# Kernel optimization log

Hardware: AMD Instinct MI355X
Metric: run time of the kernel (lower is better)

The kernel has to match this reference:

```python
import jax, jax.numpy as jnp
import numpy as np

STATE_LEN = 128
SEQ_LEN = 2048  # middle segment length; total T = SEQ_LEN + 2*STATE_LEN = 2304


def _l2norm(t):
    # matches torch F.normalize(p=2, dim=-1, eps=1e-12)
    n = jnp.sqrt(jnp.sum(t * t, axis=-1, keepdims=True))
    return t / jnp.maximum(n, 1e-12)


def setup_inputs() -> dict:
    key = jax.random.key(0)
    ks = jax.random.split(key, 8)
    B, D, H, dk, dv = 1, 1024, 16, 64, 64
    T = SEQ_LEN + 2 * STATE_LEN
    x = jax.random.normal(ks[0], (B, T, D), dtype=jnp.float32)
    w = lambda k, do: jax.random.normal(k, (H, D, do), dtype=jnp.float32) * 0.02
    return {
        "x": x,
        "Wq": w(ks[1], dk),
        "Wk": w(ks[2], dk),
        "Wv": w(ks[3], dv),
        "Wq_state": w(ks[4], dk),
        "Wk_state": w(ks[5], dk),
        "Wv_state": w(ks[6], dv),
        "scaling_factor": jnp.full((H,), 1.0 / np.sqrt(dk), dtype=jnp.float32),
    }


def reference(x, Wq, Wk, Wv, Wq_state, Wk_state, Wv_state, scaling_factor):
    sl, seq = STATE_LEN, SEQ_LEN
    # extract_state: [start_state | sequence | end_state]
    x0 = x[:, :sl]
    xm = x[:, sl:sl + seq]
    x1 = x[:, sl + seq:]

    proj = lambda t, W: jnp.einsum('bsd,hdk->bhsk', t, W)  # StackedLinear, no bias

    q = jnp.concatenate([_l2norm(proj(x0, Wq_state)), _l2norm(proj(xm, Wq)), _l2norm(proj(x1, Wq_state))], axis=2)
    k = jnp.concatenate([_l2norm(proj(x0, Wk_state)), _l2norm(proj(xm, Wk)), _l2norm(proj(x1, Wk_state))], axis=2)
    v = jnp.concatenate([_l2norm(proj(x0, Wv_state)), _l2norm(proj(xm, Wv)), _l2norm(proj(x1, Wv_state))], axis=2)

    T = q.shape[2]
    row = jnp.arange(T)[:, None]
    col = jnp.arange(T)[None, :]
    allowed = col <= row  # causal (tril, diagonal=0)
    # end-state rows may not attend to start-state cols (attn_bias[..., seq+sl:seq+2sl, :sl] = 0 before log)
    allowed = allowed & ~((row >= sl + seq) & (col < sl))
    mask = jnp.where(allowed, 0.0, -jnp.inf).astype(q.dtype)  # log of 0/1 tril

    # per-head learnable scale applied to q@k^T, then additive mask, softmax, @v
    scores = jnp.einsum('bhqd,bhkd->bhqk', q, k) * scaling_factor[None, :, None, None] + mask
    att = jax.nn.softmax(scores, axis=-1)
    return jnp.einsum('bhqk,bhkd->bhqd', att, v)
```

## Files before the change

### kernel.cpp

```cpp
#include <hip/hip_runtime.h>
#include <hip/hip_bf16.h>

#define T_TOT 2304
#define DDIM  1024
#define NH    16
#define DK    64
#define SLEN  128
#define SEQ   2048

typedef __bf16 bf16x8 __attribute__((ext_vector_type(8)));
typedef __bf16 bf16x4 __attribute__((ext_vector_type(4)));
typedef float  f32x4  __attribute__((ext_vector_type(4)));
typedef float  f32x16 __attribute__((ext_vector_type(16)));

__device__ __forceinline__ void async_copy16(const void* gsrc, void* ldst) {
  __builtin_amdgcn_global_load_lds(
      (const __attribute__((address_space(1))) void*)gsrc,
      (__attribute__((address_space(3))) void*)ldst, 16, 0, 0);
}

__device__ __forceinline__ void lds_barrier() {
  __asm__ volatile("s_waitcnt lgkmcnt(0)\n\ts_barrier" ::: "memory");
}

__global__ __launch_bounds__(256) void convert_kernel(
    const float* __restrict__ x,
    const float* __restrict__ Wq, const float* __restrict__ Wk,
    const float* __restrict__ Wv, const float* __restrict__ Wqs,
    const float* __restrict__ Wks, const float* __restrict__ Wvs,
    __bf16* __restrict__ xb, __bf16* __restrict__ Wt) {
  const int b = blockIdx.x;
  const int tid = threadIdx.x;
  if (b < 576) {
    const float4* xin = (const float4*)x;
#pragma unroll
    for (int it = 0; it < 4; ++it) {
      int idx4 = b * 1024 + it * 256 + tid;
      float4 v = xin[idx4];
      bf16x4 o;
      o[0] = (__bf16)v.x; o[1] = (__bf16)v.y; o[2] = (__bf16)v.z; o[3] = (__bf16)v.w;
      *(bf16x4*)(xb + (size_t)idx4 * 4) = o;
    }
    return;
  }
  __shared__ float tile[64 * 65];
  const int wb = b - 576;
  const int m  = wb >> 8;
  const int rem = wb & 255;
  const int h  = rem >> 4;
  const int dt = rem & 15;
  const int d0 = dt * 64;
  const float* Wsrc = (m == 0 ? Wq : m == 1 ? Wk : m == 2 ? Wv
                      : m == 3 ? Wqs : m == 4 ? Wks : Wvs) + (size_t)h * (DDIM * DK);
#pragma unroll
  for (int rr = 0; rr < 4; ++rr) {
    int drow = rr * 16 + (tid >> 4);
    int nc   = (tid & 15) * 4;
    float4 v = *(const float4*)(Wsrc + (size_t)(d0 + drow) * DK + nc);
    tile[(nc + 0) * 65 + drow] = v.x;
    tile[(nc + 1) * 65 + drow] = v.y;
    tile[(nc + 2) * 65 + drow] = v.z;
    tile[(nc + 3) * 65 + drow] = v.w;
  }
  __syncthreads();
  {
    int n  = tid >> 2;
    int rg = (tid & 3) * 16;
    __bf16* dst = Wt + (((size_t)(m * NH + h)) * DK + n) * DDIM + d0 + rg;
    bf16x8 o0, o1;
#pragma unroll
    for (int e = 0; e < 8; e++) o0[e] = (__bf16)tile[n * 65 + rg + e];
#pragma unroll
    for (int e = 0; e < 8; e++) o1[e] = (__bf16)tile[n * 65 + rg + 8 + e];
    *(bf16x8*)dst = o0;
    *(bf16x8*)(dst + 8) = o1;
  }
}

__global__ __launch_bounds__(256) void proj_kernel(
    const __bf16* __restrict__ xb, const __bf16* __restrict__ Wt,
    const float* __restrict__ scal,
    __bf16* __restrict__ qkv, __bf16* __restrict__ vt) {
  const int ntile = blockIdx.x;
  const int rt    = blockIdx.y;
  const int which = blockIdx.z;
  const int r0    = rt * 128;
  const int m     = (rt == 0 || rt == 17) ? which + 3 : which;

  __shared__ __bf16 Xs[128 * 64];
  __shared__ __bf16 Wsh[128 * 64];

  const int tid  = threadIdx.x;
  const int wave = tid >> 6, lane = tid & 63;
  const int quad = lane >> 4, lc = lane & 15;
  const int wr   = wave >> 1, wc = wave & 1;
  const int h    = ntile * 2 + wc;

  const __bf16* Wbase = Wt + ((size_t)m * NH) * (DK * DDIM) + (size_t)(ntile * 128) * DDIM;

  const f32x4 fz = {0.f, 0.f, 0.f, 0.f};
  f32x4 acc[4][4];
#pragma unroll
  for (int i = 0; i < 4; i++)
#pragma unroll
    for (int j = 0; j < 4; j++) acc[i][j] = fz;

  for (int k0 = 0; k0 < DDIM; k0 += 64) {
#pragma unroll
    for (int it = 0; it < 4; ++it) {
      int L = it * 256 + tid;
      int row = L >> 3, c = (L & 7) ^ ((L >> 3) & 7);
      async_copy16(xb + (size_t)(r0 + row) * DDIM + k0 + c * 8,
                   (char*)Xs + (size_t)(it * 256 + wave * 64) * 16);
    }
#pragma unroll
    for (int it = 0; it < 4; ++it) {
      int L = it * 256 + tid;
      int row = L >> 3, c = (L & 7) ^ ((L >> 3) & 7);
      async_copy16(Wbase + (size_t)row * DDIM + k0 + c * 8,
                   (char*)Wsh + (size_t)(it * 256 + wave * 64) * 16);
    }
    __syncthreads();
#pragma unroll
    for (int kk = 0; kk < 2; kk++) {
      bf16x8 afr[4], bfr[4];
#pragma unroll
      for (int i = 0; i < 4; i++) {
        int row = wr * 64 + i * 16 + lc;
        int ch  = (kk * 4 + quad) ^ (row & 7);
        afr[i] = *(const bf16x8*)(Xs + (row * 8 + ch) * 8);
      }
#pragma unroll
      for (int j = 0; j < 4; j++) {
        int row = wc * 64 + j * 16 + lc;
        int ch  = (kk * 4 + quad) ^ (row & 7);
        bfr[j] = *(const bf16x8*)(Wsh + (row * 8 + ch) * 8);
      }
#pragma unroll
      for (int i = 0; i < 4; i++)
#pragma unroll
        for (int j = 0; j < 4; j++)
          acc[i][j] = __builtin_amdgcn_mfma_f32_16x16x32_bf16(afr[i], bfr[j], acc[i][j], 0, 0, 0);
    }
    __syncthreads();
  }

  const float qscale = (which == 0) ? scal[h] * 1.44269504088896f : 1.0f;
  float inv4[4][4];
#pragma unroll
  for (int i = 0; i < 4; i++) {
#pragma unroll
    for (int r = 0; r < 4; r++) {
      float s = 0.f;
#pragma unroll
      for (int j = 0; j < 4; j++) { float v = acc[i][j][r]; s += v * v; }
#pragma unroll
      for (int off = 1; off < 16; off <<= 1) s += __shfl_xor(s, off, 64);
      inv4[i][r] = qscale / fmaxf(sqrtf(s), 1e-12f);
    }
  }
  if (which == 2) {
    __bf16* vtp = vt + (size_t)h * (DK * T_TOT);
#pragma unroll
    for (int i = 0; i < 4; i++) {
      int rowbase = r0 + wr * 64 + i * 16 + quad * 4;
#pragma unroll
      for (int j = 0; j < 4; j++) {
        bf16x4 o;
#pragma unroll
        for (int r = 0; r < 4; r++) o[r] = (__bf16)(acc[i][j][r] * inv4[i][r]);
        *(bf16x4*)(vtp + (size_t)(j * 16 + lc) * T_TOT + rowbase) = o;
      }
    }
  } else {
    __bf16* outp = qkv + ((size_t)(which * NH + h)) * ((size_t)T_TOT * DK);
#pragma unroll
    for (int i = 0; i < 4; i++)
#pragma unroll
      for (int r = 0; r < 4; r++) {
        int row = r0 + wr * 64 + i * 16 + quad * 4 + r;
#pragma unroll
        for (int j = 0; j < 4; j++)
          outp[(size_t)row * DK + j * 16 + lc] = (__bf16)(acc[i][j][r] * inv4[i][r]);
      }
  }
}

__global__ __launch_bounds__(256, 3) void attn_kernel(
    const __bf16* __restrict__ qkv, const __bf16* __restrict__ vt,
    float* __restrict__ Opart, float* __restrict__ Lpart) {
  const int b    = blockIdx.x;
  const int h    = b & 15;
  const int rest = b >> 4;
  const int qg   = 35 - (rest >> 1);
  const int si   = rest & 1;
  const int q0b  = qg * 64;
  const int tid  = threadIdx.x;
  const int wave = tid >> 6, lane = tid & 63;
  const int quad = lane >> 4, lc = lane & 15;
  const int l32  = lane & 31, hi = lane >> 5;

  const __bf16* qp = qkv + ((size_t)h) * ((size_t)T_TOT * DK);
  const __bf16* kp = qkv + ((size_t)(NH + h)) * ((size_t)T_TOT * DK);
  const __bf16* vp = vt + (size_t)h * (DK * T_TOT);

  __shared__ __bf16 Ks[2][64 * 64];
  __shared__ __bf16 Vs[2][64 * 64];
  __shared__ __bf16 Ps[64 * 64];
  __shared__ float  lred[4][64];

  bf16x8 qf[4][2];
#pragma unroll
  for (int qt = 0; qt < 4; qt++)
#pragma unroll
    for (int kk = 0; kk < 2; kk++)
      qf[qt][kk] = *(const bf16x8*)(qp + (size_t)(q0b + qt * 16 + lc) * DK + kk * 32 + quad * 8);

  f32x16 acc_o;
#pragma unroll
  for (int e = 0; e < 16; e++) acc_o[e] = 0.f;
  float lp[4] = {0.f, 0.f, 0.f, 0.f};

  const int jsAll = (q0b >= SLEN + SEQ) ? 2 : 0;
  const int n     = qg - jsAll + 1;
  const int half  = (n + 1) >> 1;
  const int j0    = jsAll + (si ? half : 0);
  const int j1    = si ? qg : (jsAll + half - 1);

  auto stage = [&](int j, int bufi) {
    const __bf16* kT = kp + (size_t)j * 64 * DK;
#pragma unroll
    for (int it = 0; it < 2; ++it) {
      int L = it * 256 + tid;
      int row = L >> 3, c = (L & 7) ^ ((L >> 3) & 7);
      async_copy16(kT + (size_t)row * DK + c * 8,
                   (char*)&Ks[bufi][0] + (size_t)(it * 256 + wave * 64) * 16);
    }
#pragma unroll
    for (int it = 0; it < 2; ++it) {
      int L = it * 256 + tid;
      int d = L >> 3, c = (L & 7) ^ ((L >> 3) & 7);
      async_copy16(vp + (size_t)d * T_TOT + j * 64 + c * 8,
                   (char*)&Vs[bufi][0] + (size_t)(it * 256 + wave * 64) * 16);
    }
  };

  int cur = 0;
  if (j0 <= j1) stage(j0, 0);

  const int d0 = (wave >> 1) * 32;
  const int q0 = (wave & 1) * 32;

  for (int j = j0; j <= j1; ++j) {
    __syncthreads();
    if (j < j1) stage(j + 1, cur ^ 1);

    const bool diag = (j == qg);

    bf16x8 kA[2];
#pragma unroll
    for (int kk = 0; kk < 2; kk++) {
      int row = wave * 16 + lc;
      kA[kk] = *(const bf16x8*)(&Ks[cur][(row * 8 + ((kk * 4 + quad) ^ (lc & 7))) * 8]);
    }
    f32x4 s[4];
#pragma unroll
    for (int qt = 0; qt < 4; qt++) {
      s[qt] = (f32x4){0.f, 0.f, 0.f, 0.f};
#pragma unroll
      for (int kk = 0; kk < 2; kk++)
        s[qt] = __builtin_amdgcn_mfma_f32_16x16x32_bf16(kA[kk], qf[qt][kk], s[qt], 0, 0, 0);
    }

#pragma unroll
    for (int qt = 0; qt < 4; qt++) {
      if (diag) {
#pragma unroll
        for (int r = 0; r < 4; r++)
          if ((wave * 16 + quad * 4 + r) > (qt * 16 + lc)) s[qt][r] = -__builtin_inff();
      }
      bf16x4 pb;
#pragma unroll
      for (int r = 0; r < 4; r++) {
        float pe = exp2f(s[qt][r]);
        lp[qt] += pe;
        pb[r] = (__bf16)pe;
      }
      int el = (qt * 16 + lc) * 64 + (((wave * 2 + (quad >> 1)) ^ (lc & 7)) * 8) + (quad & 1) * 4;
      *(bf16x4*)(&Ps[el]) = pb;
    }

    lds_barrier();

#pragma unroll
    for (int ks = 0; ks < 4; ks++) {
      int ch = (ks * 2 + hi) ^ (l32 & 7);
      bf16x8 vA = *(const bf16x8*)(&Vs[cur][((d0 + l32) * 8 + ch) * 8]);
      bf16x8 pB = *(const bf16x8*)(&Ps[((q0 + l32) * 8 + ch) * 8]);
      acc_o = __builtin_amdgcn_mfma_f32_32x32x16_bf16(vA, pB, acc_o, 0, 0, 0);
    }
    cur ^= 1;
  }

#pragma unroll
  for (int qt = 0; qt < 4; qt++) {
    lp[qt] += __shfl_xor(lp[qt], 16, 64);
    lp[qt] += __shfl_xor(lp[qt], 32, 64);
  }
  lred[wave][quad * 16 + lc] = lp[quad];
  __syncthreads();
  if (wave == 0)
    Lpart[(size_t)b * 64 + lane] = lred[0][lane] + lred[1][lane] + lred[2][lane] + lred[3][lane];

  float* Ob = Opart + (size_t)b * 4096;
  const size_t rowbase = (size_t)(q0 + l32) * DK;
#pragma unroll
  for (int g = 0; g < 4; g++) {
    f32x4 o;
#pragma unroll
    for (int t = 0; t < 4; t++) o[t] = acc_o[g * 4 + t];
    *(f32x4*)(&Ob[rowbase + d0 + 4 * hi + 8 * g]) = o;
  }
}

__global__ __launch_bounds__(256) void combine_kernel(
    const float* __restrict__ Opart, const float* __restrict__ Lpart,
    float* __restrict__ out) {
  const int b  = blockIdx.x;
  const int h  = b & 15;
  const int qg = b >> 4;
  const int b0 = (((35 - qg) * 2) << 4) | h;
  const int b1 = b0 + 16;
  const int tid = threadIdx.x;

  __shared__ float invl[64];
  if (tid < 64)
    invl[tid] = 1.0f / (Lpart[(size_t)b0 * 64 + tid] + Lpart[(size_t)b1 * 64 + tid]);
  __syncthreads();

  const float* O0 = Opart + (size_t)b0 * 4096;
  const float* O1 = Opart + (size_t)b1 * 4096;
  float* op = out + ((size_t)h * T_TOT + qg * 64) * DK;
#pragma unroll
  for (int it = 0; it < 4; ++it) {
    int i4 = it * 256 + tid;
    f32x4 a = *(const f32x4*)(&O0[i4 * 4]);
    f32x4 c = *(const f32x4*)(&O1[i4 * 4]);
    float iv = invl[i4 >> 4];
    f32x4 o;
#pragma unroll
    for (int r = 0; r < 4; r++) o[r] = (a[r] + c[r]) * iv;
    *(f32x4*)(&op[i4 * 4]) = o;
  }
}

extern "C" void kernel_launch(void* const* d_in, const int* in_sizes, int n_in,
                              void* d_out, int out_size, void* d_ws, size_t ws_size,
                              hipStream_t stream) {
  const float* x    = (const float*)d_in[0];
  const float* Wq   = (const float*)d_in[1];
  const float* Wk   = (const float*)d_in[2];
  const float* Wv   = (const float*)d_in[3];
  const float* Wqs  = (const float*)d_in[4];
  const float* Wks  = (const float*)d_in[5];
  const float* Wvs  = (const float*)d_in[6];
  const float* scal = (const float*)d_in[7];
  float* out = (float*)d_out;

  char* ws = (char*)d_ws;
  size_t off = 0;
  __bf16* xb    = (__bf16*)(ws + off); off += (size_t)T_TOT * DDIM * 2;
  __bf16* Wt    = (__bf16*)(ws + off); off += (size_t)6 * NH * DK * DDIM * 2;
  __bf16* qkv   = (__bf16*)(ws + off); off += (size_t)2 * NH * T_TOT * DK * 2;
  __bf16* vt    = (__bf16*)(ws + off); off += (size_t)NH * DK * T_TOT * 2;
  float*  Opart = (float*)(ws + off);  off += (size_t)1152 * 4096 * 4;
  float*  Lpart = (float*)(ws + off);

  convert_kernel<<<2112, 256, 0, stream>>>(x, Wq, Wk, Wv, Wqs, Wks, Wvs, xb, Wt);
  proj_kernel<<<dim3(8, 18, 3), 256, 0, stream>>>(xb, Wt, scal, qkv, vt);
  attn_kernel<<<dim3(1152), 256, 0, stream>>>(qkv, vt, Opart, Lpart);
  combine_kernel<<<dim3(576), 256, 0, stream>>>(Opart, Lpart, out);
}
```

Baseline: 148.9 us.

## Give each wave its own query rows in attention to drop the block barrier

The attention kernel now assigns each wave 16 query rows across all 64 keys, instead of splitting P·V across waves through a shared P tile. Each wave writes its P into a private LDS slice and reads it back without a block-wide barrier. P·V now uses 16x16x32 MFMAs over four output tiles in place of the 32x32x16 variant. Output goes through LDS staging for coalesced stores, and the row-sum reduction no longer needs a cross-wave LDS pass. In exchange each wave reads all of K and V from LDS, which raises LDS read traffic per tile.

```diff
diff --git a/kernel.cpp b/kernel.cpp
--- a/kernel.cpp
+++ b/kernel.cpp
@@ -11,16 +11,11 @@
 typedef __bf16 bf16x8 __attribute__((ext_vector_type(8)));
 typedef __bf16 bf16x4 __attribute__((ext_vector_type(4)));
 typedef float  f32x4  __attribute__((ext_vector_type(4)));
-typedef float  f32x16 __attribute__((ext_vector_type(16)));
 
 __device__ __forceinline__ void async_copy16(const void* gsrc, void* ldst) {
   __builtin_amdgcn_global_load_lds(
       (const __attribute__((address_space(1))) void*)gsrc,
       (__attribute__((address_space(3))) void*)ldst, 16, 0, 0);
-}
-
-__device__ __forceinline__ void lds_barrier() {
-  __asm__ volatile("s_waitcnt lgkmcnt(0)\n\ts_barrier" ::: "memory");
 }
 
 __global__ __launch_bounds__(256) void convert_kernel(
@@ -198,28 +193,26 @@
   const int tid  = threadIdx.x;
   const int wave = tid >> 6, lane = tid & 63;
   const int quad = lane >> 4, lc = lane & 15;
-  const int l32  = lane & 31, hi = lane >> 5;
 
   const __bf16* qp = qkv + ((size_t)h) * ((size_t)T_TOT * DK);
   const __bf16* kp = qkv + ((size_t)(NH + h)) * ((size_t)T_TOT * DK);
   const __bf16* vp = vt + (size_t)h * (DK * T_TOT);
 
-  __shared__ __bf16 Ks[2][64 * 64];
-  __shared__ __bf16 Vs[2][64 * 64];
-  __shared__ __bf16 Ps[64 * 64];
-  __shared__ float  lred[4][64];
-
-  bf16x8 qf[4][2];
-#pragma unroll
-  for (int qt = 0; qt < 4; qt++)
-#pragma unroll
-    for (int kk = 0; kk < 2; kk++)
-      qf[qt][kk] = *(const bf16x8*)(qp + (size_t)(q0b + qt * 16 + lc) * DK + kk * 32 + quad * 8);
-
-  f32x16 acc_o;
-#pragma unroll
-  for (int e = 0; e < 16; e++) acc_o[e] = 0.f;
-  float lp[4] = {0.f, 0.f, 0.f, 0.f};
+  __shared__ __align__(16) char smem[40960];
+  __bf16* Ks = (__bf16*)smem;
+  __bf16* Vs = (__bf16*)(smem + 16384);
+  __bf16* Pw = (__bf16*)(smem + 32768) + wave * 1024;
+
+  bf16x8 qf[2];
+#pragma unroll
+  for (int kk = 0; kk < 2; kk++)
+    qf[kk] = *(const bf16x8*)(qp + (size_t)(q0b + wave * 16 + lc) * DK + kk * 32 + quad * 8);
+
+  const f32x4 fz = {0.f, 0.f, 0.f, 0.f};
+  f32x4 acc[4];
+#pragma unroll
+  for (int dt = 0; dt < 4; dt++) acc[dt] = fz;
+  float lp = 0.f;
 
   const int jsAll = (q0b >= SLEN + SEQ) ? 2 : 0;
   const int n     = qg - jsAll + 1;
@@ -229,97 +222,97 @@
 
   auto stage = [&](int j, int bufi) {
     const __bf16* kT = kp + (size_t)j * 64 * DK;
+    __bf16* Kd = Ks + bufi * 4096;
+    __bf16* Vd = Vs + bufi * 4096;
 #pragma unroll
     for (int it = 0; it < 2; ++it) {
       int L = it * 256 + tid;
-      int row = L >> 3, c = (L & 7) ^ ((L >> 3) & 7);
+      int row = L >> 3, c = (L & 7) ^ (row & 7);
       async_copy16(kT + (size_t)row * DK + c * 8,
-                   (char*)&Ks[bufi][0] + (size_t)(it * 256 + wave * 64) * 16);
+                   (char*)Kd + (size_t)(it * 256 + wave * 64) * 16);
     }
 #pragma unroll
     for (int it = 0; it < 2; ++it) {
       int L = it * 256 + tid;
-      int d = L >> 3, c = (L & 7) ^ ((L >> 3) & 7);
+      int d = L >> 3, c = (L & 7) ^ (d & 7);
       async_copy16(vp + (size_t)d * T_TOT + j * 64 + c * 8,
-                   (char*)&Vs[bufi][0] + (size_t)(it * 256 + wave * 64) * 16);
+                   (char*)Vd + (size_t)(it * 256 + wave * 64) * 16);
     }
   };
 
   int cur = 0;
   if (j0 <= j1) stage(j0, 0);
-
-  const int d0 = (wave >> 1) * 32;
-  const int q0 = (wave & 1) * 32;
 
   for (int j = j0; j <= j1; ++j) {
     __syncthreads();
     if (j < j1) stage(j + 1, cur ^ 1);
 
+    const __bf16* Kc = Ks + cur * 4096;
+    const __bf16* Vc = Vs + cur * 4096;
+
+    f32x4 s[4];
+#pragma unroll
+    for (int kvt = 0; kvt < 4; kvt++) {
+      int row = kvt * 16 + lc;
+      bf16x8 a0 = *(const bf16x8*)(Kc + (row * 8 + (quad ^ (lc & 7))) * 8);
+      bf16x8 a1 = *(const bf16x8*)(Kc + (row * 8 + ((4 + quad) ^ (lc & 7))) * 8);
+      f32x4 t = __builtin_amdgcn_mfma_f32_16x16x32_bf16(a0, qf[0], fz, 0, 0, 0);
+      s[kvt]  = __builtin_amdgcn_mfma_f32_16x16x32_bf16(a1, qf[1], t, 0, 0, 0);
+    }
+
     const bool diag = (j == qg);
-
-    bf16x8 kA[2];
-#pragma unroll
-    for (int kk = 0; kk < 2; kk++) {
-      int row = wave * 16 + lc;
-      kA[kk] = *(const bf16x8*)(&Ks[cur][(row * 8 + ((kk * 4 + quad) ^ (lc & 7))) * 8]);
-    }
-    f32x4 s[4];
-#pragma unroll
-    for (int qt = 0; qt < 4; qt++) {
-      s[qt] = (f32x4){0.f, 0.f, 0.f, 0.f};
-#pragma unroll
-      for (int kk = 0; kk < 2; kk++)
-        s[qt] = __builtin_amdgcn_mfma_f32_16x16x32_bf16(kA[kk], qf[qt][kk], s[qt], 0, 0, 0);
-    }
-
-#pragma unroll
-    for (int qt = 0; qt < 4; qt++) {
+#pragma unroll
+    for (int kvt = 0; kvt < 4; kvt++) {
       if (diag) {
 #pragma unroll
         for (int r = 0; r < 4; r++)
-          if ((wave * 16 + quad * 4 + r) > (qt * 16 + lc)) s[qt][r] = -__builtin_inff();
+          if ((kvt * 16 + quad * 4 + r) > (wave * 16 + lc)) s[kvt][r] = -__builtin_inff();
       }
       bf16x4 pb;
 #pragma unroll
       for (int r = 0; r < 4; r++) {
-        float pe = exp2f(s[qt][r]);
-        lp[qt] += pe;
+        float pe = exp2f(s[kvt][r]);
+        lp += pe;
         pb[r] = (__bf16)pe;
       }
-      int el = (qt * 16 + lc) * 64 + (((wave * 2 + (quad >> 1)) ^ (lc & 7)) * 8) + (quad & 1) * 4;
-      *(bf16x4*)(&Ps[el]) = pb;
-    }
-
-    lds_barrier();
-
-#pragma unroll
-    for (int ks = 0; ks < 4; ks++) {
-      int ch = (ks * 2 + hi) ^ (l32 & 7);
-      bf16x8 vA = *(const bf16x8*)(&Vs[cur][((d0 + l32) * 8 + ch) * 8]);
-      bf16x8 pB = *(const bf16x8*)(&Ps[((q0 + l32) * 8 + ch) * 8]);
-      acc_o = __builtin_amdgcn_mfma_f32_32x32x16_bf16(vA, pB, acc_o, 0, 0, 0);
+      int c = (kvt * 4 + quad) ^ ((lc & 7) << 1);
+      *(bf16x4*)(Pw + lc * 64 + c * 4) = pb;
+    }
+
+    bf16x8 pB[2];
+#pragma unroll
+    for (int kk = 0; kk < 2; kk++)
+      pB[kk] = *(const bf16x8*)(Pw + lc * 64 + ((kk * 8 + quad * 2) ^ ((lc & 7) << 1)) * 4);
+#pragma unroll
+    for (int dt = 0; dt < 4; dt++) {
+      int row = dt * 16 + lc;
+#pragma unroll
+      for (int kk = 0; kk < 2; kk++) {
+        bf16x8 vA = *(const bf16x8*)(Vc + (row * 8 + ((kk * 4 + quad) ^ (lc & 7))) * 8);
+        acc[dt] = __builtin_amdgcn_mfma_f32_16x16x32_bf16(vA, pB[kk], acc[dt], 0, 0, 0);
+      }
     }
     cur ^= 1;
   }
 
-#pragma unroll
-  for (int qt = 0; qt < 4; qt++) {
-    lp[qt] += __shfl_xor(lp[qt], 16, 64);
-    lp[qt] += __shfl_xor(lp[qt], 32, 64);
-  }
-  lred[wave][quad * 16 + lc] = lp[quad];
+  lp += __shfl_xor(lp, 16, 64);
+  lp += __shfl_xor(lp, 32, 64);
+  if (lane < 16) Lpart[(size_t)b * 64 + wave * 16 + lane] = lp;
+
   __syncthreads();
-  if (wave == 0)
-    Lpart[(size_t)b * 64 + lane] = lred[0][lane] + lred[1][lane] + lred[2][lane] + lred[3][lane];
+  float* Ot = (float*)smem + wave * (16 * 68);
+#pragma unroll
+  for (int dt = 0; dt < 4; dt++)
+#pragma unroll
+    for (int r = 0; r < 4; r++)
+      Ot[lc * 68 + dt * 16 + quad * 4 + r] = acc[dt][r];
 
   float* Ob = Opart + (size_t)b * 4096;
-  const size_t rowbase = (size_t)(q0 + l32) * DK;
+  const int q2 = lane >> 2, dsg = (lane & 3) * 16;
 #pragma unroll
   for (int g = 0; g < 4; g++) {
-    f32x4 o;
-#pragma unroll
-    for (int t = 0; t < 4; t++) o[t] = acc_o[g * 4 + t];
-    *(f32x4*)(&Ob[rowbase + d0 + 4 * hi + 8 * g]) = o;
+    f32x4 v = *(const f32x4*)(&Ot[q2 * 68 + dsg + g * 4]);
+    *(f32x4*)(&Ob[(size_t)(wave * 16 + q2) * 64 + dsg + g * 4]) = v;
   }
 }
 
```

New measurement: 145.1 us. 1.03x faster.
